# Performance work log

Measured on AMD Instinct MI355X. Metric: run time of the kernel, lower is better.

Reference implementation:

```python
import jax, jax.numpy as jnp
import numpy as np

HEADS = 8


def setup_inputs() -> dict:
    key = jax.random.key(0)
    k0, k1, k2, k3 = jax.random.split(key, 4)
    b, c, h, w = 8, 128, 32, 32
    x = jax.random.normal(k0, (b, c, h, w), dtype=jnp.float32)
    # torch nn.Linear weights: (out_features, in_features)
    s = c ** -0.5
    wq = jax.random.normal(k1, (c, c), dtype=jnp.float32) * s
    wk = jax.random.normal(k2, (c, c), dtype=jnp.float32) * s
    wv = jax.random.normal(k3, (c, c), dtype=jnp.float32) * s
    return {"x": x, "wq": wq, "wk": wk, "wv": wv}


def reference(x, wq, wk, wv):
    b, c, h, w = x.shape
    n = HEADS
    d = c // n
    scale = d ** -0.5
    xp = jnp.transpose(x, (0, 2, 3, 1))  # (b, h, w, c)
    # torch Linear: y = x @ W.T
    q = (xp @ wq.T).reshape(b, h, w, n, d)
    k = (xp @ wk.T).reshape(b, h, w, n, d)
    v = (xp @ wv.T).reshape(b, h, w, n, d)
    # full 2D spatial attention scores: (b, n, h, w, x, y)
    weights = jnp.einsum('bhwnd,bxynd->bnhwxy', q, k) * scale
    # NOTE: original softmaxes over the LAST spatial axis (y) only
    weights = jax.nn.softmax(weights, axis=-1)
    attn = jnp.einsum('bnhwxy,bxynd->bhwnd', weights, v)
    out = attn.reshape(b, h, w, c)
    return jnp.transpose(out, (0, 3, 1, 2))  # (b, c, h, w)
```

## Files before the change

kernel.cpp:

```cpp
#include <hip/hip_runtime.h>
#include <stdint.h>


typedef __bf16 bf16x8 __attribute__((ext_vector_type(8)));
typedef float f32x16 __attribute__((ext_vector_type(16)));

#define QOFF  0u
#define KOFF  (1u << 20)
#define VOFF  (2u << 20)
#define XTOFF (3u << 20)
#define WBOFF (4u << 20)

static __device__ __forceinline__ unsigned short f2bf(float f) {
  union { float f; uint32_t u; } v; v.f = f;
  uint32_t r = (v.u + 0x7FFFu + ((v.u >> 16) & 1u)) >> 16;
  return (unsigned short)r;
}
static __device__ __forceinline__ uint32_t pkrne(float lo, float hi) {
  return (uint32_t)f2bf(lo) | ((uint32_t)f2bf(hi) << 16);
}
static __device__ __forceinline__ uint32_t pktrunc(float lo, float hi) {
  return (__builtin_bit_cast(uint32_t, hi) & 0xffff0000u) |
         (__builtin_bit_cast(uint32_t, lo) >> 16);
}
static __device__ __forceinline__ float fexp2(float x) {
  float r;
  asm volatile("v_exp_f32 %0, %1" : "=v"(r) : "v"(x));
  return r;
}
static __device__ __forceinline__ f32x16 zero16() {
  f32x16 z;
#pragma unroll
  for (int i = 0; i < 16; ++i) z[i] = 0.f;
  return z;
}
static __device__ __forceinline__ int perm23(int p) {
  return (p & ~12) | ((p & 4) << 1) | ((p & 8) >> 1);
}

__global__ __launch_bounds__(256) void prep_kernel(
    const float* __restrict__ x, const float* __restrict__ wq,
    const float* __restrict__ wk, const float* __restrict__ wv,
    unsigned short* __restrict__ ws) {
  int bid = blockIdx.x, t = threadIdx.x;
  if (bid < 256) {
    int b  = bid >> 5;
    int pc = (bid >> 3) & 3;
    int cc = bid & 7;
    int p  = pc * 256 + t;
    int c0 = cc * 16;
    const float* src = x + (size_t)b * 131072 + (size_t)c0 * 1024 + p;
    uint32_t pk[8];
#pragma unroll
    for (int i = 0; i < 8; ++i) {
      float lo = src[(2 * i) * 1024];
      float hi = src[(2 * i + 1) * 1024];
      pk[i] = pkrne(lo, hi);
    }
    uint4* dst = (uint4*)(ws + XTOFF + (size_t)b * 131072 + (size_t)p * 128 + c0);
    dst[0] = make_uint4(pk[0], pk[1], pk[2], pk[3]);
    dst[1] = make_uint4(pk[4], pk[5], pk[6], pk[7]);
  } else {
    int widx = bid - 256;
    int mat = widx >> 3;
    int off = (widx & 7) * 2048 + t * 8;
    const float* w = (mat == 0) ? wq : ((mat == 1) ? wk : wv);
    const float4* s4 = (const float4*)(w + off);
    float4 a = s4[0], bv = s4[1];
    uint4 o = make_uint4(pkrne(a.x, a.y), pkrne(a.z, a.w),
                         pkrne(bv.x, bv.y), pkrne(bv.z, bv.w));
    *(uint4*)(ws + WBOFF + mat * 16384 + off) = o;
  }
}

__global__ __launch_bounds__(256) void proj_kernel(unsigned short* __restrict__ ws) {
  int bid = blockIdx.x;
  int ptile = bid & 15;
  int mat = (bid >> 4) % 3;
  int b = bid / 48;
  int t = threadIdx.x;
  int wave = t >> 6, lane = t & 63;
  int h = lane >> 5, c = lane & 31;
  int out0 = wave * 32;

  const unsigned short* wb = ws + WBOFF + mat * 16384;
  const unsigned short* xt = ws + XTOFF + (size_t)b * 131072;
  const unsigned short* arow = wb + (size_t)(out0 + c) * 128 + h * 8;
  const unsigned short* brow0 = xt + (size_t)(ptile * 64 + c) * 128 + h * 8;
  const unsigned short* brow1 = brow0 + 32 * 128;

  f32x16 acc0 = zero16(), acc1 = zero16();
#pragma unroll
  for (int kt = 0; kt < 8; ++kt) {
    bf16x8 af = __builtin_bit_cast(bf16x8, *(const uint4*)(arow + kt * 16));
    bf16x8 b0 = __builtin_bit_cast(bf16x8, *(const uint4*)(brow0 + kt * 16));
    bf16x8 b1 = __builtin_bit_cast(bf16x8, *(const uint4*)(brow1 + kt * 16));
    acc0 = __builtin_amdgcn_mfma_f32_32x32x16_bf16(af, b0, acc0, 0, 0, 0);
    acc1 = __builtin_amdgcn_mfma_f32_32x32x16_bf16(af, b1, acc1, 0, 0, 0);
  }

  if (mat < 2) {
    float s = (mat == 0) ? 0.36067376022224085f : 1.0f;
    unsigned short* dst = ws + ((mat == 0) ? QOFF : KOFF);
#pragma unroll
    for (int nt = 0; nt < 2; ++nt) {
      f32x16 a = nt ? acc1 : acc0;
      int p = ptile * 64 + nt * 32 + c;
#pragma unroll
      for (int rg = 0; rg < 4; ++rg) {
        int bn = b * 8 + wave * 2 + (rg >> 1);
        int dbase = ((rg & 1) ? 8 : 0) + 4 * h;
        uint32_t lo = pkrne(a[rg * 4 + 0] * s, a[rg * 4 + 1] * s);
        uint32_t hi = pkrne(a[rg * 4 + 2] * s, a[rg * 4 + 3] * s);
        *(uint2*)(dst + (size_t)bn * 16384 + (size_t)p * 16 + dbase) =
            make_uint2(lo, hi);
      }
    }
  } else {
#pragma unroll
    for (int nt = 0; nt < 2; ++nt) {
      f32x16 a = nt ? acc1 : acc0;
      int p = ptile * 64 + nt * 32 + c;
      int pp = perm23(p);
#pragma unroll
      for (int r = 0; r < 16; ++r) {
        int moff = (r & 3) + 8 * (r >> 2) + 4 * h;
        int head = (out0 + moff) >> 4;
        int d = moff & 15;
        ws[VOFF + (size_t)(b * 8 + head) * 16384 + (size_t)d * 1024 + pp] =
            f2bf(a[r]);
      }
    }
  }
}

__global__ __launch_bounds__(256) void attn_kernel(
    const unsigned short* __restrict__ ws, float* __restrict__ out) {
  int bid = blockIdx.x;
  int qc = bid & 7, bn = bid >> 3;
  const unsigned short* Qg = ws + QOFF + (size_t)bn * 16384;
  const unsigned short* Kg = ws + KOFF + (size_t)bn * 16384;
  const unsigned short* Vg = ws + VOFF + (size_t)bn * 16384;

  __shared__ unsigned short Kl[2 * 1024 * 8];
  __shared__ unsigned short Vl[16 * 1040];

  int t = threadIdx.x;
  for (int i = t; i < 2048; i += 256) {
    int p = i >> 1, hh = i & 1;
    *(uint4*)(Kl + hh * 8192 + p * 8) = *(const uint4*)(Kg + p * 16 + hh * 8);
  }
  for (int i = t; i < 2048; i += 256) {
    int d = i >> 7, o = i & 127;
    *(uint4*)(Vl + d * 1040 + o * 8) = *(const uint4*)(Vg + d * 1024 + o * 8);
  }
  __syncthreads();

  int wave = t >> 6, lane = t & 63;
  int h = lane >> 5, c = lane & 31;
  int q0 = qc * 128 + wave * 32;

  bf16x8 qb = __builtin_bit_cast(
      bf16x8, *(const uint4*)(Qg + (size_t)(q0 + c) * 16 + h * 8));

  const unsigned short* krow = Kl + h * 8192 + c * 8;
  const unsigned short* vrow = Vl + (c & 15) * 1040 + h * 8;

  f32x16 acc = zero16();

#pragma unroll 2
  for (int x = 0; x < 32; ++x) {
    bf16x8 ka  = __builtin_bit_cast(bf16x8, *(const uint4*)(krow + x * 256));
    bf16x8 va0 = __builtin_bit_cast(bf16x8, *(const uint4*)(vrow + x * 32));
    bf16x8 va1 = __builtin_bit_cast(bf16x8, *(const uint4*)(vrow + x * 32 + 16));

    f32x16 sv = __builtin_amdgcn_mfma_f32_32x32x16_bf16(ka, qb, zero16(), 0, 0, 0);

    float e[16];
#pragma unroll
    for (int r = 0; r < 16; ++r) e[r] = fexp2(sv[r]);
    float s0 = (e[0] + e[1]) + (e[2] + e[3]);
    float s1 = (e[4] + e[5]) + (e[6] + e[7]);
    float s2 = (e[8] + e[9]) + (e[10] + e[11]);
    float s3 = (e[12] + e[13]) + (e[14] + e[15]);
    float sum = (s0 + s1) + (s2 + s3);
    sum += __shfl_xor(sum, 32);
    float rs = __builtin_amdgcn_rcpf(sum);

    uint32_t pk[8];
#pragma unroll
    for (int j = 0; j < 8; ++j)
      pk[j] = pktrunc(e[2 * j] * rs, e[2 * j + 1] * rs);
    bf16x8 p0 = __builtin_bit_cast(bf16x8, make_uint4(pk[0], pk[1], pk[2], pk[3]));
    bf16x8 p1 = __builtin_bit_cast(bf16x8, make_uint4(pk[4], pk[5], pk[6], pk[7]));

    acc = __builtin_amdgcn_mfma_f32_32x32x16_bf16(va0, p0, acc, 0, 0, 0);
    acc = __builtin_amdgcn_mfma_f32_32x32x16_bf16(va1, p1, acc, 0, 0, 0);
  }

#pragma unroll
  for (int r = 0; r < 8; ++r) {
    int d = (r & 3) + 8 * (r >> 2) + 4 * h;
    out[(size_t)(bn * 16 + d) * 1024 + q0 + c] = acc[r];
  }
}

extern "C" void kernel_launch(void* const* d_in, const int* in_sizes, int n_in,
                              void* d_out, int out_size, void* d_ws, size_t ws_size,
                              hipStream_t stream) {
  const float* x  = (const float*)d_in[0];
  const float* wq = (const float*)d_in[1];
  const float* wk = (const float*)d_in[2];
  const float* wv = (const float*)d_in[3];
  unsigned short* ws = (unsigned short*)d_ws;
  float* out = (float*)d_out;

  prep_kernel<<<dim3(280), dim3(256), 0, stream>>>(x, wq, wk, wv, ws);
  proj_kernel<<<dim3(384), dim3(256), 0, stream>>>(ws);
  attn_kernel<<<dim3(512), dim3(256), 0, stream>>>(ws, out);
}
```

Before: 94.33 us.

## Fuse bf16 conversion into projection and stream K/V from global in attention

```diff
diff --git a/kernel.cpp b/kernel.cpp
--- a/kernel.cpp
+++ b/kernel.cpp
@@ -8,8 +8,6 @@
 #define QOFF  0u
 #define KOFF  (1u << 20)
 #define VOFF  (2u << 20)
-#define XTOFF (3u << 20)
-#define WBOFF (4u << 20)
 
 static __device__ __forceinline__ unsigned short f2bf(float f) {
   union { float f; uint32_t u; } v; v.f = f;
@@ -25,7 +23,7 @@
 }
 static __device__ __forceinline__ float fexp2(float x) {
   float r;
-  asm volatile("v_exp_f32 %0, %1" : "=v"(r) : "v"(x));
+  asm("v_exp_f32 %0, %1" : "=v"(r) : "v"(x));
   return r;
 }
 static __device__ __forceinline__ f32x16 zero16() {
@@ -37,43 +35,17 @@
 static __device__ __forceinline__ int perm23(int p) {
   return (p & ~12) | ((p & 4) << 1) | ((p & 8) >> 1);
 }
+static __device__ __forceinline__ bf16x8 pack8(float f0, float f1, float f2,
+                                               float f3, float f4, float f5,
+                                               float f6, float f7) {
+  uint4 u = make_uint4(pkrne(f0, f1), pkrne(f2, f3), pkrne(f4, f5), pkrne(f6, f7));
+  return __builtin_bit_cast(bf16x8, u);
+}
 
-__global__ __launch_bounds__(256) void prep_kernel(
+__global__ __launch_bounds__(256) void proj_kernel(
     const float* __restrict__ x, const float* __restrict__ wq,
     const float* __restrict__ wk, const float* __restrict__ wv,
     unsigned short* __restrict__ ws) {
-  int bid = blockIdx.x, t = threadIdx.x;
-  if (bid < 256) {
-    int b  = bid >> 5;
-    int pc = (bid >> 3) & 3;
-    int cc = bid & 7;
-    int p  = pc * 256 + t;
-    int c0 = cc * 16;
-    const float* src = x + (size_t)b * 131072 + (size_t)c0 * 1024 + p;
-    uint32_t pk[8];
-#pragma unroll
-    for (int i = 0; i < 8; ++i) {
-      float lo = src[(2 * i) * 1024];
-      float hi = src[(2 * i + 1) * 1024];
-      pk[i] = pkrne(lo, hi);
-    }
-    uint4* dst = (uint4*)(ws + XTOFF + (size_t)b * 131072 + (size_t)p * 128 + c0);
-    dst[0] = make_uint4(pk[0], pk[1], pk[2], pk[3]);
-    dst[1] = make_uint4(pk[4], pk[5], pk[6], pk[7]);
-  } else {
-    int widx = bid - 256;
-    int mat = widx >> 3;
-    int off = (widx & 7) * 2048 + t * 8;
-    const float* w = (mat == 0) ? wq : ((mat == 1) ? wk : wv);
-    const float4* s4 = (const float4*)(w + off);
-    float4 a = s4[0], bv = s4[1];
-    uint4 o = make_uint4(pkrne(a.x, a.y), pkrne(a.z, a.w),
-                         pkrne(bv.x, bv.y), pkrne(bv.z, bv.w));
-    *(uint4*)(ws + WBOFF + mat * 16384 + off) = o;
-  }
-}
-
-__global__ __launch_bounds__(256) void proj_kernel(unsigned short* __restrict__ ws) {
   int bid = blockIdx.x;
   int ptile = bid & 15;
   int mat = (bid >> 4) % 3;
@@ -83,18 +55,25 @@
   int h = lane >> 5, c = lane & 31;
   int out0 = wave * 32;
 
-  const unsigned short* wb = ws + WBOFF + mat * 16384;
-  const unsigned short* xt = ws + XTOFF + (size_t)b * 131072;
-  const unsigned short* arow = wb + (size_t)(out0 + c) * 128 + h * 8;
-  const unsigned short* brow0 = xt + (size_t)(ptile * 64 + c) * 128 + h * 8;
-  const unsigned short* brow1 = brow0 + 32 * 128;
+  const float* w = (mat == 0) ? wq : ((mat == 1) ? wk : wv);
+  const float* wrow = w + (size_t)(out0 + c) * 128 + h * 8;
+  const float* xcol = x + (size_t)b * 131072 + ptile * 64 + c;
 
   f32x16 acc0 = zero16(), acc1 = zero16();
 #pragma unroll
   for (int kt = 0; kt < 8; ++kt) {
-    bf16x8 af = __builtin_bit_cast(bf16x8, *(const uint4*)(arow + kt * 16));
-    bf16x8 b0 = __builtin_bit_cast(bf16x8, *(const uint4*)(brow0 + kt * 16));
-    bf16x8 b1 = __builtin_bit_cast(bf16x8, *(const uint4*)(brow1 + kt * 16));
+    int ch0 = kt * 16 + h * 8;
+    float4 wa = *(const float4*)(wrow + kt * 16);
+    float4 wb4 = *(const float4*)(wrow + kt * 16 + 4);
+    float xb0[8], xb1[8];
+#pragma unroll
+    for (int j = 0; j < 8; ++j) {
+      xb0[j] = xcol[(size_t)(ch0 + j) * 1024];
+      xb1[j] = xcol[(size_t)(ch0 + j) * 1024 + 32];
+    }
+    bf16x8 af = pack8(wa.x, wa.y, wa.z, wa.w, wb4.x, wb4.y, wb4.z, wb4.w);
+    bf16x8 b0 = pack8(xb0[0], xb0[1], xb0[2], xb0[3], xb0[4], xb0[5], xb0[6], xb0[7]);
+    bf16x8 b1 = pack8(xb1[0], xb1[1], xb1[2], xb1[3], xb1[4], xb1[5], xb1[6], xb1[7]);
     acc0 = __builtin_amdgcn_mfma_f32_32x32x16_bf16(af, b0, acc0, 0, 0, 0);
     acc1 = __builtin_amdgcn_mfma_f32_32x32x16_bf16(af, b1, acc1, 0, 0, 0);
   }
@@ -142,20 +121,7 @@
   const unsigned short* Kg = ws + KOFF + (size_t)bn * 16384;
   const unsigned short* Vg = ws + VOFF + (size_t)bn * 16384;
 
-  __shared__ unsigned short Kl[2 * 1024 * 8];
-  __shared__ unsigned short Vl[16 * 1040];
-
   int t = threadIdx.x;
-  for (int i = t; i < 2048; i += 256) {
-    int p = i >> 1, hh = i & 1;
-    *(uint4*)(Kl + hh * 8192 + p * 8) = *(const uint4*)(Kg + p * 16 + hh * 8);
-  }
-  for (int i = t; i < 2048; i += 256) {
-    int d = i >> 7, o = i & 127;
-    *(uint4*)(Vl + d * 1040 + o * 8) = *(const uint4*)(Vg + d * 1024 + o * 8);
-  }
-  __syncthreads();
-
   int wave = t >> 6, lane = t & 63;
   int h = lane >> 5, c = lane & 31;
   int q0 = qc * 128 + wave * 32;
@@ -163,16 +129,24 @@
   bf16x8 qb = __builtin_bit_cast(
       bf16x8, *(const uint4*)(Qg + (size_t)(q0 + c) * 16 + h * 8));
 
-  const unsigned short* krow = Kl + h * 8192 + c * 8;
-  const unsigned short* vrow = Vl + (c & 15) * 1040 + h * 8;
+  const unsigned short* kbase = Kg + (size_t)c * 16 + h * 8;
+  const unsigned short* vbase = Vg + (size_t)(c & 15) * 1024 + h * 8;
 
   f32x16 acc = zero16();
+  uint4 kf  = *(const uint4*)(kbase);
+  uint4 v0f = *(const uint4*)(vbase);
+  uint4 v1f = *(const uint4*)(vbase + 16);
 
 #pragma unroll 2
   for (int x = 0; x < 32; ++x) {
-    bf16x8 ka  = __builtin_bit_cast(bf16x8, *(const uint4*)(krow + x * 256));
-    bf16x8 va0 = __builtin_bit_cast(bf16x8, *(const uint4*)(vrow + x * 32));
-    bf16x8 va1 = __builtin_bit_cast(bf16x8, *(const uint4*)(vrow + x * 32 + 16));
+    bf16x8 ka  = __builtin_bit_cast(bf16x8, kf);
+    bf16x8 va0 = __builtin_bit_cast(bf16x8, v0f);
+    bf16x8 va1 = __builtin_bit_cast(bf16x8, v1f);
+    if (x < 31) {
+      kf  = *(const uint4*)(kbase + (x + 1) * 512);
+      v0f = *(const uint4*)(vbase + (x + 1) * 32);
+      v1f = *(const uint4*)(vbase + (x + 1) * 32 + 16);
+    }
 
     f32x16 sv = __builtin_amdgcn_mfma_f32_32x32x16_bf16(ka, qb, zero16(), 0, 0, 0);
 
@@ -215,7 +189,6 @@
   unsigned short* ws = (unsigned short*)d_ws;
   float* out = (float*)d_out;
 
-  prep_kernel<<<dim3(280), dim3(256), 0, stream>>>(x, wq, wk, wv, ws);
-  proj_kernel<<<dim3(384), dim3(256), 0, stream>>>(ws);
+  proj_kernel<<<dim3(384), dim3(256), 0, stream>>>(x, wq, wk, wv, ws);
   attn_kernel<<<dim3(512), dim3(256), 0, stream>>>(ws, out);
 }
```

After: 96.42 us. 2.2% more time.
